# Optimization experiments

Measured on AMD Instinct MI355X. Metric: run time of the kernel, lower is better.

The kernel has to match this reference:

```python
import jax, jax.numpy as jnp
import numpy as np

LN2 = float(np.log(2.0))

def ssp(x):
    # ShiftedSoftplus: softplus(x) - log(2)
    return jax.nn.softplus(x) - LN2

N_NODES = 40000
N_EDGES = 640000
HIDDEN = 128
N_FILTERS = 128
N_GAUSS = 50
CUTOFF = 10.0

def setup_inputs() -> dict:
    key = jax.random.key(0)
    ks = jax.random.split(key, 12)
    s = 0.05
    x = jax.random.normal(ks[0], (N_NODES, HIDDEN), dtype=jnp.float32)
    edge_index = jax.random.randint(ks[1], (2, N_EDGES), 0, N_NODES)
    edge_weight = jax.random.uniform(ks[2], (N_EDGES,), dtype=jnp.float32) * CUTOFF
    edge_attr = jax.random.normal(ks[3], (N_EDGES, N_GAUSS), dtype=jnp.float32)
    # filter MLP params (Linear(num_gaussians,num_filters), ssp, Linear(num_filters,num_filters))
    mlp_w1 = jax.random.normal(ks[4], (N_FILTERS, N_GAUSS), dtype=jnp.float32) * s
    mlp_b1 = jnp.zeros((N_FILTERS,), dtype=jnp.float32)
    mlp_w2 = jax.random.normal(ks[5], (N_FILTERS, N_FILTERS), dtype=jnp.float32) * s
    mlp_b2 = jnp.zeros((N_FILTERS,), dtype=jnp.float32)
    # CFConv linears: lin1 (no bias), lin2 (bias)
    lin1_w = jax.random.normal(ks[6], (N_FILTERS, HIDDEN), dtype=jnp.float32) * s
    lin2_w = jax.random.normal(ks[7], (HIDDEN, N_FILTERS), dtype=jnp.float32) * s
    lin2_b = jnp.zeros((HIDDEN,), dtype=jnp.float32)
    # output linear
    lin_w = jax.random.normal(ks[8], (HIDDEN, HIDDEN), dtype=jnp.float32) * s
    lin_b = jnp.zeros((HIDDEN,), dtype=jnp.float32)
    return {
        "x": x, "edge_index": edge_index, "edge_weight": edge_weight, "edge_attr": edge_attr,
        "mlp_w1": mlp_w1, "mlp_b1": mlp_b1, "mlp_w2": mlp_w2, "mlp_b2": mlp_b2,
        "lin1_w": lin1_w, "lin2_w": lin2_w, "lin2_b": lin2_b,
        "lin_w": lin_w, "lin_b": lin_b,
    }

def reference(x, edge_index, edge_weight, edge_attr,
              mlp_w1, mlp_b1, mlp_w2, mlp_b2,
              lin1_w, lin2_w, lin2_b, lin_w, lin_b):
    src, dst = edge_index[0], edge_index[1]
    # cosine envelope
    C = 0.5 * (jnp.cos(edge_weight * jnp.pi / CUTOFF) + 1.0)  # (E,)
    # filter MLP on Gaussian-smeared distances
    W = ssp(edge_attr @ mlp_w1.T + mlp_b1) @ mlp_w2.T + mlp_b2  # (E, F)
    W = W * C[:, None]
    # CFConv: lin1 -> gather x_j -> multiply -> scatter-add -> lin2
    h = x @ lin1_w.T                                            # (N, F)
    msg = h[src] * W                                            # (E, F)
    agg = jax.ops.segment_sum(msg, dst, num_segments=x.shape[0])  # (N, F)
    h2 = agg @ lin2_w.T + lin2_b                                # (N, H)
    # activation + output projection
    out = ssp(h2) @ lin_w.T + lin_b                             # (N, H)
    return out
```

## Files before the change

### kernel.cpp

```cpp
#include <hip/hip_runtime.h>
#include <math.h>

#define LN2F 0.69314718055994531f

typedef _Float16 v8hf __attribute__((ext_vector_type(8)));
typedef float    v4f  __attribute__((ext_vector_type(4)));

__device__ __forceinline__ float ssp_fast(float x) {
    float e = __expf(-fabsf(x));
    return fmaxf(x, 0.f) + __logf(1.f + e) - LN2F;
}

__global__ __launch_bounds__(256)
void prep_kernel(const float* __restrict__ w1, const float* __restrict__ w2,
                 const float* __restrict__ l1w, const float* __restrict__ l2w,
                 const float* __restrict__ lw,
                 _Float16* __restrict__ w1f, _Float16* __restrict__ w2f,
                 _Float16* __restrict__ l1f, _Float16* __restrict__ l2f,
                 _Float16* __restrict__ lwf)
{
    int idx = blockIdx.x * 256 + threadIdx.x;
    if (idx < 8192) {
        int i = idx & 7, lane = (idx >> 3) & 63, ks = (idx >> 9) & 1, nt = idx >> 10;
        int r = nt * 16 + (lane & 15);
        int k = ks * 32 + (lane >> 4) * 8 + i;
        w1f[idx] = (k < 50) ? (_Float16)w1[r * 50 + k] : (_Float16)0.f;
        return;
    }
    int o = idx - 8192;
    if (o >= 4 * 16384) return;
    int which = o >> 14;
    int p = o & 16383;
    int i = p & 7, lane = (p >> 3) & 63, ks = (p >> 9) & 3, nt = p >> 11;
    int r = nt * 16 + (lane & 15);
    int k = ks * 32 + (lane >> 4) * 8 + i;
    const float* src = (which == 0) ? w2 : (which == 1) ? l1w : (which == 2) ? l2w : lw;
    _Float16* dst   = (which == 0) ? w2f : (which == 1) ? l1f : (which == 2) ? l2f : lwf;
    dst[p] = (_Float16)src[r * 128 + k];
}

__global__ __launch_bounds__(256)
void h_gemm_kernel(const float* __restrict__ X, const _Float16* __restrict__ Wf,
                   float* __restrict__ Y, int M)
{
    const int tid = threadIdx.x, lane = tid & 63, wv = tid >> 6;
    const int l15 = lane & 15, quad = lane >> 4;
    const int mb = blockIdx.x * 64 + wv * 16;
    const int nt0 = blockIdx.y * 4;

    const int mA = (mb + l15 < M) ? (mb + l15) : (M - 1);
    v8hf a[4];
    #pragma unroll
    for (int ks = 0; ks < 4; ++ks) {
        const float4* xp = (const float4*)&X[(size_t)mA * 128 + ks * 32 + quad * 8];
        float4 x0 = xp[0], x1 = xp[1];
        v8hf t = {(_Float16)x0.x, (_Float16)x0.y, (_Float16)x0.z, (_Float16)x0.w,
                  (_Float16)x1.x, (_Float16)x1.y, (_Float16)x1.z, (_Float16)x1.w};
        a[ks] = t;
    }
    #pragma unroll
    for (int nt = nt0; nt < nt0 + 4; ++nt) {
        v4f acc = {0.f, 0.f, 0.f, 0.f};
        #pragma unroll
        for (int ks = 0; ks < 4; ++ks) {
            const v8hf b = *(const v8hf*)&Wf[((nt * 4 + ks) * 64 + lane) * 8];
            acc = __builtin_amdgcn_mfma_f32_16x16x32_f16(a[ks], b, acc, 0, 0, 0);
        }
        const int col = nt * 16 + l15;
        #pragma unroll
        for (int r = 0; r < 4; ++r) {
            int row = mb + quad * 4 + r;
            if (row < M) Y[(size_t)row * 128 + col] = acc[r];
        }
    }
}

__global__ __launch_bounds__(256)
void fused_out_kernel(const float* __restrict__ agg, const _Float16* __restrict__ l2f,
                      const float* __restrict__ l2b, const _Float16* __restrict__ lwf,
                      const float* __restrict__ lb, float* __restrict__ out, int M)
{
    __shared__ __align__(16) _Float16 Sh[64 * 138];
    const int tid = threadIdx.x, lane = tid & 63, wv = tid >> 6;
    const int l15 = lane & 15, quad = lane >> 4;
    const int m0 = wv * 16;
    const int gbase = blockIdx.x * 64;
    const int nt0 = blockIdx.y * 4;

    const int mA = (gbase + m0 + l15 < M) ? (gbase + m0 + l15) : (M - 1);
    v8hf a[4];
    #pragma unroll
    for (int ks = 0; ks < 4; ++ks) {
        const float4* xp = (const float4*)&agg[(size_t)mA * 128 + ks * 32 + quad * 8];
        float4 x0 = xp[0], x1 = xp[1];
        v8hf t = {(_Float16)x0.x, (_Float16)x0.y, (_Float16)x0.z, (_Float16)x0.w,
                  (_Float16)x1.x, (_Float16)x1.y, (_Float16)x1.z, (_Float16)x1.w};
        a[ks] = t;
    }
    #pragma unroll
    for (int nt = 0; nt < 8; ++nt) {
        v4f acc = {0.f, 0.f, 0.f, 0.f};
        #pragma unroll
        for (int ks = 0; ks < 4; ++ks) {
            const v8hf b = *(const v8hf*)&l2f[((nt * 4 + ks) * 64 + lane) * 8];
            acc = __builtin_amdgcn_mfma_f32_16x16x32_f16(a[ks], b, acc, 0, 0, 0);
        }
        const float bj = l2b[nt * 16 + l15];
        #pragma unroll
        for (int r = 0; r < 4; ++r)
            Sh[(m0 + quad * 4 + r) * 138 + nt * 16 + l15] =
                (_Float16)ssp_fast(acc[r] + bj);
    }
    v8hf ua[4];
    #pragma unroll
    for (int ks = 0; ks < 4; ++ks)
        ua[ks] = *(const v8hf*)&Sh[(m0 + l15) * 138 + ks * 32 + quad * 8];

    #pragma unroll
    for (int nt = nt0; nt < nt0 + 4; ++nt) {
        v4f acc = {0.f, 0.f, 0.f, 0.f};
        #pragma unroll
        for (int ks = 0; ks < 4; ++ks) {
            const v8hf b = *(const v8hf*)&lwf[((nt * 4 + ks) * 64 + lane) * 8];
            acc = __builtin_amdgcn_mfma_f32_16x16x32_f16(ua[ks], b, acc, 0, 0, 0);
        }
        const int col = nt * 16 + l15;
        const float bj = lb[col];
        #pragma unroll
        for (int r = 0; r < 4; ++r) {
            int row = gbase + m0 + quad * 4 + r;
            if (row < M) out[(size_t)row * 128 + col] = acc[r] + bj;
        }
    }
}

__global__ __launch_bounds__(256)
void attr16_kernel(const float* __restrict__ attr, _Float16* __restrict__ attrL, int E)
{
    int idx = blockIdx.x * 256 + threadIdx.x;
    const int stride = gridDim.x * 256;
    const int total = E * 8;
    for (; idx < total; idx += stride) {
        const int e = idx >> 3, sub = idx & 7;
        const float* rp = attr + (size_t)e * 50 + sub * 8;
        v8hf t;
        #pragma unroll
        for (int j = 0; j < 8; ++j) {
            const int c = sub * 8 + j;
            t[j] = (c < 50) ? (_Float16)rp[j] : (_Float16)0.f;
        }
        *(v8hf*)&attrL[(size_t)e * 64 + sub * 8] = t;
    }
}

__global__ __launch_bounds__(256)
void rank_hist_kernel(const int* __restrict__ dst, int* __restrict__ cnt,
                      int* __restrict__ rank, int E)
{
    int i = blockIdx.x * 256 + threadIdx.x;
    const int stride = gridDim.x * 256;
    for (; i < E; i += stride) rank[i] = atomicAdd(&cnt[dst[i]], 1);
}

__global__ __launch_bounds__(256)
void scan1_kernel(int* __restrict__ data, int* __restrict__ bsum, int N)
{
    __shared__ int wsum[4];
    const int t = threadIdx.x, lane = t & 63, wv = t >> 6;
    const int base = blockIdx.x * 1024 + t * 4;
    int v0 = 0, v1 = 0, v2 = 0, v3 = 0;
    if (base + 0 < N) v0 = data[base + 0];
    if (base + 1 < N) v1 = data[base + 1];
    if (base + 2 < N) v2 = data[base + 2];
    if (base + 3 < N) v3 = data[base + 3];
    const int s = v0 + v1 + v2 + v3;
    int sc = s;
    #pragma unroll
    for (int d = 1; d < 64; d <<= 1) {
        int o = __shfl_up(sc, d);
        if (lane >= d) sc += o;
    }
    if (lane == 63) wsum[wv] = sc;
    __syncthreads();
    int wo = 0;
    for (int j = 0; j < wv; ++j) wo += wsum[j];
    int run = wo + (sc - s);
    if (base + 0 < N) data[base + 0] = run; run += v0;
    if (base + 1 < N) data[base + 1] = run; run += v1;
    if (base + 2 < N) data[base + 2] = run; run += v2;
    if (base + 3 < N) data[base + 3] = run; run += v3;
    if (t == 255) bsum[blockIdx.x] = wo + sc;
}

__global__ __launch_bounds__(256)
void scan2_kernel(int* __restrict__ offs, const int* __restrict__ bsum, int N, int E)
{
    int add = 0;
    for (int j = 0; j < (int)blockIdx.x; ++j) add += bsum[j];
    const int base = blockIdx.x * 1024 + threadIdx.x * 4;
    #pragma unroll
    for (int r = 0; r < 4; ++r) {
        int i = base + r;
        if (i < N) offs[i] += add;
    }
    if (blockIdx.x == 0 && threadIdx.x == 0) offs[N] = E;
}

__global__ __launch_bounds__(256)
void build_rec_kernel(const int* __restrict__ src, const int* __restrict__ dst,
                      const float* __restrict__ ew, const int* __restrict__ rank,
                      const int* __restrict__ offs, int4* __restrict__ recP, int E)
{
    int i = blockIdx.x * 256 + threadIdx.x;
    const int stride = gridDim.x * 256;
    for (; i < E; i += stride) {
        const int d = dst[i];
        const int slot = offs[d] + rank[i];
        int4 rec;
        rec.x = i;
        rec.y = src[i];
        rec.z = d;
        rec.w = __float_as_int(0.5f * (__cosf(ew[i] * 0.31415926535897932f) + 1.f));
        recP[slot] = rec;
    }
}

__global__ __launch_bounds__(256, 7)
void edge_kernel(const _Float16* __restrict__ attrL,
                 const int4* __restrict__ recP,
                 const _Float16* __restrict__ w1f,
                 const _Float16* __restrict__ w2f,
                 const float* __restrict__ b1,
                 const float* __restrict__ b2,
                 const float* __restrict__ h,
                 float* __restrict__ agg,
                 int E)
{
    __shared__ __align__(16) _Float16 Uh[64 * 138];

    const int tid = threadIdx.x;
    const int e_base = blockIdx.x * 64;
    const int lane = tid & 63, wv = tid >> 6;
    const int m0 = wv * 16, l15 = lane & 15, quad = lane >> 4;

    const int s0 = e_base + m0 + quad * 4;
    int dIdx[4]; float cC[4]; const float* hrow[4]; float* arow[4]; bool val[4];
    #pragma unroll
    for (int r = 0; r < 4; ++r) {
        const int sg = s0 + r;
        val[r] = sg < E;
        const int s = val[r] ? sg : (E - 1);
        const int4 rec = recP[s];
        dIdx[r] = rec.z;
        cC[r] = __int_as_float(rec.w);
        hrow[r] = h + (size_t)rec.y * 128;
        arow[r] = agg + (size_t)rec.z * 128;
    }

    int sA = e_base + m0 + l15;
    if (sA >= E) sA = E - 1;
    const int eidA = ((const int*)recP)[(size_t)sA * 4];
    const _Float16* ap = attrL + (size_t)eidA * 64;
    const v8hf a0 = *(const v8hf*)(ap + quad * 8);
    const v8hf a1 = *(const v8hf*)(ap + 32 + quad * 8);

    float hv[8][4];
    #pragma unroll
    for (int nt = 0; nt < 8; ++nt)
        #pragma unroll
        for (int r = 0; r < 4; ++r)
            hv[nt][r] = hrow[r][nt * 16 + l15];

    #pragma unroll
    for (int nt = 0; nt < 8; ++nt) {
        v4f acc = {0.f, 0.f, 0.f, 0.f};
        const v8hf bA = *(const v8hf*)&w1f[((nt * 2 + 0) * 64 + lane) * 8];
        const v8hf bB = *(const v8hf*)&w1f[((nt * 2 + 1) * 64 + lane) * 8];
        acc = __builtin_amdgcn_mfma_f32_16x16x32_f16(a0, bA, acc, 0, 0, 0);
        acc = __builtin_amdgcn_mfma_f32_16x16x32_f16(a1, bB, acc, 0, 0, 0);
        const float bj = b1[nt * 16 + l15];
        #pragma unroll
        for (int r = 0; r < 4; ++r)
            Uh[(m0 + quad * 4 + r) * 138 + nt * 16 + l15] =
                (_Float16)ssp_fast(acc[r] + bj);
    }

    v8hf ua[4];
    #pragma unroll
    for (int ks = 0; ks < 4; ++ks)
        ua[ks] = *(const v8hf*)&Uh[(m0 + l15) * 138 + ks * 32 + quad * 8];

    #pragma unroll
    for (int nt = 0; nt < 8; ++nt) {
        v4f acc = {0.f, 0.f, 0.f, 0.f};
        #pragma unroll
        for (int ks = 0; ks < 4; ++ks) {
            const v8hf b = *(const v8hf*)&w2f[((nt * 4 + ks) * 64 + lane) * 8];
            acc = __builtin_amdgcn_mfma_f32_16x16x32_f16(ua[ks], b, acc, 0, 0, 0);
        }
        const int col = nt * 16 + l15;
        const float bj = b2[col];
        float m[4];
        #pragma unroll
        for (int r = 0; r < 4; ++r)
            m[r] = val[r] ? (acc[r] + bj) * cC[r] * hv[nt][r] : 0.f;
        float run = m[0];
        #pragma unroll
        for (int r = 1; r < 4; ++r) {
            if (dIdx[r] == dIdx[r - 1]) {
                run += m[r];
            } else {
                atomicAdd(arow[r - 1] + col, run);
                run = m[r];
            }
        }
        atomicAdd(arow[3] + col, run);
    }
}

extern "C" void kernel_launch(void* const* d_in, const int* in_sizes, int n_in,
                              void* d_out, int out_size, void* d_ws, size_t ws_size,
                              hipStream_t stream)
{
    const float* x   = (const float*)d_in[0];
    const int*   ei  = (const int*)  d_in[1];
    const float* ew  = (const float*)d_in[2];
    const float* ea  = (const float*)d_in[3];
    const float* w1  = (const float*)d_in[4];
    const float* b1  = (const float*)d_in[5];
    const float* w2  = (const float*)d_in[6];
    const float* b2  = (const float*)d_in[7];
    const float* l1w = (const float*)d_in[8];
    const float* l2w = (const float*)d_in[9];
    const float* l2b = (const float*)d_in[10];
    const float* lw  = (const float*)d_in[11];
    const float* lb  = (const float*)d_in[12];

    const int N = in_sizes[0] / 128;
    const int E = in_sizes[2];
    const int NB = (N + 1023) / 1024;

    char* base = (char*)d_ws;
    size_t off = 0;
    auto take = [&](size_t bytes) -> char* {
        char* r = base + off;
        off = (off + bytes + 255) & ~(size_t)255;
        return r;
    };
    float*    hbuf  = (float*)   take((size_t)N * 128 * 4);
    float*    agg   = (float*)   take((size_t)N * 128 * 4);
    _Float16* w1f   = (_Float16*)take(8192 * 2);
    _Float16* w2f   = (_Float16*)take(16384 * 2);
    _Float16* l1f   = (_Float16*)take(16384 * 2);
    _Float16* l2f   = (_Float16*)take(16384 * 2);
    _Float16* lwf   = (_Float16*)take(16384 * 2);
    int*      offs  = (int*)     take((size_t)(N + 1) * 4);
    int*      bsum  = (int*)     take((size_t)NB * 4);
    int*      rank  = (int*)     take((size_t)E * 4);
    int4*     recP  = (int4*)    take((size_t)E * 16);
    _Float16* attrL = (_Float16*)take((size_t)E * 64 * 2);

    const int nb = (N + 63) / 64;
    const int eb = (E + 63) / 64;
    const int tb = (E + 255) / 256;

    prep_kernel<<<288, 256, 0, stream>>>(w1, w2, l1w, l2w, lw,
                                         w1f, w2f, l1f, l2f, lwf);
    hipMemsetAsync(agg, 0, (size_t)N * 128 * sizeof(float), stream);
    hipMemsetAsync(offs, 0, (size_t)(N + 1) * sizeof(int), stream);

    attr16_kernel<<<(E * 8 + 255) / 256, 256, 0, stream>>>(ea, attrL, E);
    rank_hist_kernel<<<tb, 256, 0, stream>>>(ei + E, offs, rank, E);
    scan1_kernel<<<NB, 256, 0, stream>>>(offs, bsum, N);
    scan2_kernel<<<NB, 256, 0, stream>>>(offs, bsum, N, E);
    build_rec_kernel<<<tb, 256, 0, stream>>>(ei, ei + E, ew, rank, offs, recP, E);

    h_gemm_kernel<<<dim3(nb, 2), 256, 0, stream>>>(x, l1f, hbuf, N);
    edge_kernel<<<eb, 256, 0, stream>>>(attrL, recP, w1f, w2f, b1, b2,
                                        hbuf, agg, E);
    fused_out_kernel<<<dim3(nb, 2), 256, 0, stream>>>(agg, l2f, l2b, lwf, lb,
                                                      (float*)d_out, N);
}
```

Baseline: 575.2 us.

## Make edge kernel persistent with W2 held in registers and W1 in LDS

Turns the edge kernel into a persistent grid of 512 blocks that loop over 64-edge tiles. Each block loads W1 into shared memory and each lane keeps its W2 fragments (32 v8hf) and the biases in registers once, instead of re-reading them from global memory per tile. Launch bounds drop from 7 to 2 blocks per SM so the much larger register footprint fits. The cost is lower occupancy and less latency hiding for the irregular h gathers and atomics.

```diff
diff --git a/kernel.cpp b/kernel.cpp
--- a/kernel.cpp
+++ b/kernel.cpp
@@ -225,7 +225,7 @@
     }
 }
 
-__global__ __launch_bounds__(256, 7)
+__global__ __launch_bounds__(256, 2)
 void edge_kernel(const _Float16* __restrict__ attrL,
                  const int4* __restrict__ recP,
                  const _Float16* __restrict__ w1f,
@@ -234,87 +234,107 @@
                  const float* __restrict__ b2,
                  const float* __restrict__ h,
                  float* __restrict__ agg,
-                 int E)
-{
+                 int E, int nTiles)
+{
+    __shared__ __align__(16) _Float16 W1s[8192];
     __shared__ __align__(16) _Float16 Uh[64 * 138];
 
     const int tid = threadIdx.x;
-    const int e_base = blockIdx.x * 64;
     const int lane = tid & 63, wv = tid >> 6;
     const int m0 = wv * 16, l15 = lane & 15, quad = lane >> 4;
 
-    const int s0 = e_base + m0 + quad * 4;
-    int dIdx[4]; float cC[4]; const float* hrow[4]; float* arow[4]; bool val[4];
-    #pragma unroll
-    for (int r = 0; r < 4; ++r) {
-        const int sg = s0 + r;
-        val[r] = sg < E;
-        const int s = val[r] ? sg : (E - 1);
-        const int4 rec = recP[s];
-        dIdx[r] = rec.z;
-        cC[r] = __int_as_float(rec.w);
-        hrow[r] = h + (size_t)rec.y * 128;
-        arow[r] = agg + (size_t)rec.z * 128;
-    }
-
-    int sA = e_base + m0 + l15;
-    if (sA >= E) sA = E - 1;
-    const int eidA = ((const int*)recP)[(size_t)sA * 4];
-    const _Float16* ap = attrL + (size_t)eidA * 64;
-    const v8hf a0 = *(const v8hf*)(ap + quad * 8);
-    const v8hf a1 = *(const v8hf*)(ap + 32 + quad * 8);
-
-    float hv[8][4];
-    #pragma unroll
-    for (int nt = 0; nt < 8; ++nt)
-        #pragma unroll
-        for (int r = 0; r < 4; ++r)
-            hv[nt][r] = hrow[r][nt * 16 + l15];
-
+    #pragma unroll
+    for (int i = 0; i < 4; ++i)
+        ((v8hf*)W1s)[tid + 256 * i] = ((const v8hf*)w1f)[tid + 256 * i];
+
+    v8hf w2r[32];
+    #pragma unroll
+    for (int f = 0; f < 32; ++f)
+        w2r[f] = *(const v8hf*)&w2f[((size_t)f * 64 + lane) * 8];
+
+    float b1v[8], b2v[8];
     #pragma unroll
     for (int nt = 0; nt < 8; ++nt) {
-        v4f acc = {0.f, 0.f, 0.f, 0.f};
-        const v8hf bA = *(const v8hf*)&w1f[((nt * 2 + 0) * 64 + lane) * 8];
-        const v8hf bB = *(const v8hf*)&w1f[((nt * 2 + 1) * 64 + lane) * 8];
-        acc = __builtin_amdgcn_mfma_f32_16x16x32_f16(a0, bA, acc, 0, 0, 0);
-        acc = __builtin_amdgcn_mfma_f32_16x16x32_f16(a1, bB, acc, 0, 0, 0);
-        const float bj = b1[nt * 16 + l15];
-        #pragma unroll
-        for (int r = 0; r < 4; ++r)
-            Uh[(m0 + quad * 4 + r) * 138 + nt * 16 + l15] =
-                (_Float16)ssp_fast(acc[r] + bj);
-    }
-
-    v8hf ua[4];
-    #pragma unroll
-    for (int ks = 0; ks < 4; ++ks)
-        ua[ks] = *(const v8hf*)&Uh[(m0 + l15) * 138 + ks * 32 + quad * 8];
-
-    #pragma unroll
-    for (int nt = 0; nt < 8; ++nt) {
-        v4f acc = {0.f, 0.f, 0.f, 0.f};
-        #pragma unroll
-        for (int ks = 0; ks < 4; ++ks) {
-            const v8hf b = *(const v8hf*)&w2f[((nt * 4 + ks) * 64 + lane) * 8];
-            acc = __builtin_amdgcn_mfma_f32_16x16x32_f16(ua[ks], b, acc, 0, 0, 0);
-        }
-        const int col = nt * 16 + l15;
-        const float bj = b2[col];
-        float m[4];
-        #pragma unroll
-        for (int r = 0; r < 4; ++r)
-            m[r] = val[r] ? (acc[r] + bj) * cC[r] * hv[nt][r] : 0.f;
-        float run = m[0];
-        #pragma unroll
-        for (int r = 1; r < 4; ++r) {
-            if (dIdx[r] == dIdx[r - 1]) {
-                run += m[r];
-            } else {
-                atomicAdd(arow[r - 1] + col, run);
-                run = m[r];
+        b1v[nt] = b1[nt * 16 + l15];
+        b2v[nt] = b2[nt * 16 + l15];
+    }
+    __syncthreads();
+
+    for (int tile = blockIdx.x; tile < nTiles; tile += (int)gridDim.x) {
+        const int e_base = tile * 64;
+
+        const int s0 = e_base + m0 + quad * 4;
+        int dIdx[4]; float cC[4]; const float* hrow[4]; float* arow[4]; bool val[4];
+        #pragma unroll
+        for (int r = 0; r < 4; ++r) {
+            const int sg = s0 + r;
+            val[r] = sg < E;
+            const int s = val[r] ? sg : (E - 1);
+            const int4 rec = recP[s];
+            dIdx[r] = rec.z;
+            cC[r] = __int_as_float(rec.w);
+            hrow[r] = h + (size_t)rec.y * 128;
+            arow[r] = agg + (size_t)rec.z * 128;
+        }
+
+        int sA = e_base + m0 + l15;
+        if (sA >= E) sA = E - 1;
+        const int eidA = ((const int*)recP)[(size_t)sA * 4];
+        const _Float16* ap = attrL + (size_t)eidA * 64;
+        const v8hf a0 = *(const v8hf*)(ap + quad * 8);
+        const v8hf a1 = *(const v8hf*)(ap + 32 + quad * 8);
+
+        float hv[8][4];
+        #pragma unroll
+        for (int nt = 0; nt < 8; ++nt)
+            #pragma unroll
+            for (int r = 0; r < 4; ++r)
+                hv[nt][r] = hrow[r][nt * 16 + l15];
+
+        #pragma unroll
+        for (int nt = 0; nt < 8; ++nt) {
+            v4f acc = {0.f, 0.f, 0.f, 0.f};
+            const v8hf bA = *(const v8hf*)&W1s[((nt * 2 + 0) * 64 + lane) * 8];
+            const v8hf bB = *(const v8hf*)&W1s[((nt * 2 + 1) * 64 + lane) * 8];
+            acc = __builtin_amdgcn_mfma_f32_16x16x32_f16(a0, bA, acc, 0, 0, 0);
+            acc = __builtin_amdgcn_mfma_f32_16x16x32_f16(a1, bB, acc, 0, 0, 0);
+            const float bj = b1v[nt];
+            #pragma unroll
+            for (int r = 0; r < 4; ++r)
+                Uh[(m0 + quad * 4 + r) * 138 + nt * 16 + l15] =
+                    (_Float16)ssp_fast(acc[r] + bj);
+        }
+
+        v8hf ua[4];
+        #pragma unroll
+        for (int ks = 0; ks < 4; ++ks)
+            ua[ks] = *(const v8hf*)&Uh[(m0 + l15) * 138 + ks * 32 + quad * 8];
+
+        #pragma unroll
+        for (int nt = 0; nt < 8; ++nt) {
+            v4f acc = {0.f, 0.f, 0.f, 0.f};
+            #pragma unroll
+            for (int ks = 0; ks < 4; ++ks)
+                acc = __builtin_amdgcn_mfma_f32_16x16x32_f16(ua[ks], w2r[nt * 4 + ks],
+                                                             acc, 0, 0, 0);
+            const int col = nt * 16 + l15;
+            const float bj = b2v[nt];
+            float m[4];
+            #pragma unroll
+            for (int r = 0; r < 4; ++r)
+                m[r] = val[r] ? (acc[r] + bj) * cC[r] * hv[nt][r] : 0.f;
+            float run = m[0];
+            #pragma unroll
+            for (int r = 1; r < 4; ++r) {
+                if (dIdx[r] == dIdx[r - 1]) {
+                    run += m[r];
+                } else {
+                    atomicAdd(arow[r - 1] + col, run);
+                    run = m[r];
+                }
             }
-        }
-        atomicAdd(arow[3] + col, run);
+            atomicAdd(arow[3] + col, run);
+        }
     }
 }
 
@@ -361,8 +381,8 @@
     _Float16* attrL = (_Float16*)take((size_t)E * 64 * 2);
 
     const int nb = (N + 63) / 64;
-    const int eb = (E + 63) / 64;
     const int tb = (E + 255) / 256;
+    const int nTiles = (E + 63) / 64;
 
     prep_kernel<<<288, 256, 0, stream>>>(w1, w2, l1w, l2w, lw,
                                          w1f, w2f, l1f, l2f, lwf);
@@ -376,8 +396,8 @@
     build_rec_kernel<<<tb, 256, 0, stream>>>(ei, ei + E, ew, rank, offs, recP, E);
 
     h_gemm_kernel<<<dim3(nb, 2), 256, 0, stream>>>(x, l1f, hbuf, N);
-    edge_kernel<<<eb, 256, 0, stream>>>(attrL, recP, w1f, w2f, b1, b2,
-                                        hbuf, agg, E);
+    edge_kernel<<<512, 256, 0, stream>>>(attrL, recP, w1f, w2f, b1, b2,
+                                         hbuf, agg, E, nTiles);
     fused_out_kernel<<<dim3(nb, 2), 256, 0, stream>>>(agg, l2f, l2b, lwf, lb,
                                                       (float*)d_out, N);
 }
```

Measured after the change: 569.7 us. Within noise of the previous version (-1.0%).

## Fuse attr fp16 conversion with edge permutation into dst-sorted layout

Applied to the files above, without the earlier changes.

The separate attr16 and build_rec kernels are merged into one perm_kernel. It converts edge_attr to fp16 and writes it directly at the dst-sorted slot, alongside the edge record. The edge kernel then reads attributes contiguously by sorted position instead of gathering them through the original edge id. This removes one launch and the indirect gather, but the attr writes become scattered. Separately, h_gemm uses 4 column blocks of 2 tiles each for more parallelism, and edge_kernel's occupancy hint rises to 8.

```diff
diff --git a/kernel.cpp b/kernel.cpp
--- a/kernel.cpp
+++ b/kernel.cpp
@@ -46,7 +46,7 @@
     const int tid = threadIdx.x, lane = tid & 63, wv = tid >> 6;
     const int l15 = lane & 15, quad = lane >> 4;
     const int mb = blockIdx.x * 64 + wv * 16;
-    const int nt0 = blockIdx.y * 4;
+    const int nt0 = blockIdx.y * 2;
 
     const int mA = (mb + l15 < M) ? (mb + l15) : (M - 1);
     v8hf a[4];
@@ -59,7 +59,7 @@
         a[ks] = t;
     }
     #pragma unroll
-    for (int nt = nt0; nt < nt0 + 4; ++nt) {
+    for (int nt = nt0; nt < nt0 + 2; ++nt) {
         v4f acc = {0.f, 0.f, 0.f, 0.f};
         #pragma unroll
         for (int ks = 0; ks < 4; ++ks) {
@@ -131,25 +131,6 @@
             int row = gbase + m0 + quad * 4 + r;
             if (row < M) out[(size_t)row * 128 + col] = acc[r] + bj;
         }
-    }
-}
-
-__global__ __launch_bounds__(256)
-void attr16_kernel(const float* __restrict__ attr, _Float16* __restrict__ attrL, int E)
-{
-    int idx = blockIdx.x * 256 + threadIdx.x;
-    const int stride = gridDim.x * 256;
-    const int total = E * 8;
-    for (; idx < total; idx += stride) {
-        const int e = idx >> 3, sub = idx & 7;
-        const float* rp = attr + (size_t)e * 50 + sub * 8;
-        v8hf t;
-        #pragma unroll
-        for (int j = 0; j < 8; ++j) {
-            const int c = sub * 8 + j;
-            t[j] = (c < 50) ? (_Float16)rp[j] : (_Float16)0.f;
-        }
-        *(v8hf*)&attrL[(size_t)e * 64 + sub * 8] = t;
     }
 }
 
@@ -207,26 +188,39 @@
 }
 
 __global__ __launch_bounds__(256)
-void build_rec_kernel(const int* __restrict__ src, const int* __restrict__ dst,
-                      const float* __restrict__ ew, const int* __restrict__ rank,
-                      const int* __restrict__ offs, int4* __restrict__ recP, int E)
-{
-    int i = blockIdx.x * 256 + threadIdx.x;
+void perm_kernel(const float* __restrict__ attr, const float* __restrict__ ew,
+                 const int* __restrict__ src, const int* __restrict__ dst,
+                 const int* __restrict__ rank, const int* __restrict__ offs,
+                 int4* __restrict__ recP, _Float16* __restrict__ attrP, int E)
+{
+    int idx = blockIdx.x * 256 + threadIdx.x;
     const int stride = gridDim.x * 256;
-    for (; i < E; i += stride) {
-        const int d = dst[i];
-        const int slot = offs[d] + rank[i];
-        int4 rec;
-        rec.x = i;
-        rec.y = src[i];
-        rec.z = d;
-        rec.w = __float_as_int(0.5f * (__cosf(ew[i] * 0.31415926535897932f) + 1.f));
-        recP[slot] = rec;
-    }
-}
-
-__global__ __launch_bounds__(256, 7)
-void edge_kernel(const _Float16* __restrict__ attrL,
+    const int total = E * 8;
+    for (; idx < total; idx += stride) {
+        const int e = idx >> 3, sub = idx & 7;
+        const int d = dst[e];
+        const int slot = offs[d] + rank[e];
+        const float* rp = attr + (size_t)e * 50 + sub * 8;
+        v8hf t;
+        #pragma unroll
+        for (int j = 0; j < 8; ++j) {
+            const int c = sub * 8 + j;
+            t[j] = (c < 50) ? (_Float16)rp[j] : (_Float16)0.f;
+        }
+        *(v8hf*)&attrP[(size_t)slot * 64 + sub * 8] = t;
+        if (sub == 0) {
+            int4 rec;
+            rec.x = src[e];
+            rec.y = d;
+            rec.z = __float_as_int(0.5f * (__cosf(ew[e] * 0.31415926535897932f) + 1.f));
+            rec.w = 0;
+            recP[slot] = rec;
+        }
+    }
+}
+
+__global__ __launch_bounds__(256, 8)
+void edge_kernel(const _Float16* __restrict__ attrP,
                  const int4* __restrict__ recP,
                  const _Float16* __restrict__ w1f,
                  const _Float16* __restrict__ w2f,
@@ -251,16 +245,15 @@
         val[r] = sg < E;
         const int s = val[r] ? sg : (E - 1);
         const int4 rec = recP[s];
-        dIdx[r] = rec.z;
-        cC[r] = __int_as_float(rec.w);
-        hrow[r] = h + (size_t)rec.y * 128;
-        arow[r] = agg + (size_t)rec.z * 128;
+        dIdx[r] = rec.y;
+        cC[r] = __int_as_float(rec.z);
+        hrow[r] = h + (size_t)rec.x * 128;
+        arow[r] = agg + (size_t)rec.y * 128;
     }
 
     int sA = e_base + m0 + l15;
     if (sA >= E) sA = E - 1;
-    const int eidA = ((const int*)recP)[(size_t)sA * 4];
-    const _Float16* ap = attrL + (size_t)eidA * 64;
+    const _Float16* ap = attrP + (size_t)sA * 64;
     const v8hf a0 = *(const v8hf*)(ap + quad * 8);
     const v8hf a1 = *(const v8hf*)(ap + 32 + quad * 8);
 
@@ -358,7 +351,7 @@
     int*      bsum  = (int*)     take((size_t)NB * 4);
     int*      rank  = (int*)     take((size_t)E * 4);
     int4*     recP  = (int4*)    take((size_t)E * 16);
-    _Float16* attrL = (_Float16*)take((size_t)E * 64 * 2);
+    _Float16* attrP = (_Float16*)take((size_t)E * 64 * 2);
 
     const int nb = (N + 63) / 64;
     const int eb = (E + 63) / 64;
@@ -369,14 +362,14 @@
     hipMemsetAsync(agg, 0, (size_t)N * 128 * sizeof(float), stream);
     hipMemsetAsync(offs, 0, (size_t)(N + 1) * sizeof(int), stream);
 
-    attr16_kernel<<<(E * 8 + 255) / 256, 256, 0, stream>>>(ea, attrL, E);
     rank_hist_kernel<<<tb, 256, 0, stream>>>(ei + E, offs, rank, E);
     scan1_kernel<<<NB, 256, 0, stream>>>(offs, bsum, N);
     scan2_kernel<<<NB, 256, 0, stream>>>(offs, bsum, N, E);
-    build_rec_kernel<<<tb, 256, 0, stream>>>(ei, ei + E, ew, rank, offs, recP, E);
-
-    h_gemm_kernel<<<dim3(nb, 2), 256, 0, stream>>>(x, l1f, hbuf, N);
-    edge_kernel<<<eb, 256, 0, stream>>>(attrL, recP, w1f, w2f, b1, b2,
+    perm_kernel<<<(E * 8 + 255) / 256, 256, 0, stream>>>(ea, ew, ei, ei + E,
+                                                         rank, offs, recP, attrP, E);
+
+    h_gemm_kernel<<<dim3(nb, 4), 256, 0, stream>>>(x, l1f, hbuf, N);
+    edge_kernel<<<eb, 256, 0, stream>>>(attrP, recP, w1f, w2f, b1, b2,
                                         hbuf, agg, E);
     fused_out_kernel<<<dim3(nb, 2), 256, 0, stream>>>(agg, l2f, l2b, lwf, lb,
                                                       (float*)d_out, N);
```

New measurement: 608.6 us. 1.06x slower.

## Merge preprocessing kernels into one cooperative grid-synced build kernel

Applied to the files above, without the earlier changes.

Replaces the separate prep, memset, attr conversion, histogram, two-pass scan and record-build launches with a single cooperative kernel of 512 blocks that uses grid.sync between phases. The aim is to remove launch and inter-kernel gap overhead across about eight small launches. The trade-off is grid-wide barriers, a serial bsum scan on one thread, and fewer threads for the bandwidth-bound phases. It also raises the edge kernel's launch_bounds occupancy hint from 7 to 8, and keeps the old multi-kernel path as a fallback if the cooperative launch fails.

```diff
diff --git a/kernel.cpp b/kernel.cpp
--- a/kernel.cpp
+++ b/kernel.cpp
@@ -1,5 +1,8 @@
 #include <hip/hip_runtime.h>
+#include <hip/hip_cooperative_groups.h>
 #include <math.h>
+
+namespace cg = cooperative_groups;
 
 #define LN2F 0.69314718055994531f
 
@@ -11,15 +14,14 @@
     return fmaxf(x, 0.f) + __logf(1.f + e) - LN2F;
 }
 
-__global__ __launch_bounds__(256)
-void prep_kernel(const float* __restrict__ w1, const float* __restrict__ w2,
-                 const float* __restrict__ l1w, const float* __restrict__ l2w,
-                 const float* __restrict__ lw,
-                 _Float16* __restrict__ w1f, _Float16* __restrict__ w2f,
-                 _Float16* __restrict__ l1f, _Float16* __restrict__ l2f,
-                 _Float16* __restrict__ lwf)
-{
-    int idx = blockIdx.x * 256 + threadIdx.x;
+__device__ __forceinline__ void prep_unit(int idx,
+    const float* __restrict__ w1, const float* __restrict__ w2,
+    const float* __restrict__ l1w, const float* __restrict__ l2w,
+    const float* __restrict__ lw,
+    _Float16* __restrict__ w1f, _Float16* __restrict__ w2f,
+    _Float16* __restrict__ l1f, _Float16* __restrict__ l2f,
+    _Float16* __restrict__ lwf)
+{
     if (idx < 8192) {
         int i = idx & 7, lane = (idx >> 3) & 63, ks = (idx >> 9) & 1, nt = idx >> 10;
         int r = nt * 16 + (lane & 15);
@@ -39,99 +41,119 @@
     dst[p] = (_Float16)src[r * 128 + k];
 }
 
-__global__ __launch_bounds__(256)
-void h_gemm_kernel(const float* __restrict__ X, const _Float16* __restrict__ Wf,
-                   float* __restrict__ Y, int M)
-{
-    const int tid = threadIdx.x, lane = tid & 63, wv = tid >> 6;
-    const int l15 = lane & 15, quad = lane >> 4;
-    const int mb = blockIdx.x * 64 + wv * 16;
-    const int nt0 = blockIdx.y * 4;
-
-    const int mA = (mb + l15 < M) ? (mb + l15) : (M - 1);
-    v8hf a[4];
-    #pragma unroll
-    for (int ks = 0; ks < 4; ++ks) {
-        const float4* xp = (const float4*)&X[(size_t)mA * 128 + ks * 32 + quad * 8];
-        float4 x0 = xp[0], x1 = xp[1];
-        v8hf t = {(_Float16)x0.x, (_Float16)x0.y, (_Float16)x0.z, (_Float16)x0.w,
-                  (_Float16)x1.x, (_Float16)x1.y, (_Float16)x1.z, (_Float16)x1.w};
-        a[ks] = t;
-    }
-    #pragma unroll
-    for (int nt = nt0; nt < nt0 + 4; ++nt) {
-        v4f acc = {0.f, 0.f, 0.f, 0.f};
-        #pragma unroll
-        for (int ks = 0; ks < 4; ++ks) {
-            const v8hf b = *(const v8hf*)&Wf[((nt * 4 + ks) * 64 + lane) * 8];
-            acc = __builtin_amdgcn_mfma_f32_16x16x32_f16(a[ks], b, acc, 0, 0, 0);
-        }
-        const int col = nt * 16 + l15;
+__device__ __forceinline__ void attr_unit(int idx, const float* __restrict__ attr,
+                                          _Float16* __restrict__ attrL)
+{
+    const int e = idx >> 3, sub = idx & 7;
+    const float* rp = attr + (size_t)e * 50 + sub * 8;
+    v8hf t;
+    #pragma unroll
+    for (int j = 0; j < 8; ++j) {
+        const int c = sub * 8 + j;
+        t[j] = (c < 50) ? (_Float16)rp[j] : (_Float16)0.f;
+    }
+    *(v8hf*)&attrL[(size_t)e * 64 + sub * 8] = t;
+}
+
+__global__ __launch_bounds__(256)
+void build_kernel(const float* __restrict__ attr, const float* __restrict__ ew,
+                  const int* __restrict__ src, const int* __restrict__ dst,
+                  const float* __restrict__ w1, const float* __restrict__ w2,
+                  const float* __restrict__ l1w, const float* __restrict__ l2w,
+                  const float* __restrict__ lw,
+                  _Float16* __restrict__ w1f, _Float16* __restrict__ w2f,
+                  _Float16* __restrict__ l1f, _Float16* __restrict__ l2f,
+                  _Float16* __restrict__ lwf,
+                  int* __restrict__ cnt, int* __restrict__ rank,
+                  int* __restrict__ bsum, int4* __restrict__ recP,
+                  _Float16* __restrict__ attrL, float* __restrict__ agg,
+                  int N, int E, int nChunks)
+{
+    cg::grid_group grid = cg::this_grid();
+    const int gtid = blockIdx.x * 256 + threadIdx.x;
+    const int gstride = gridDim.x * 256;
+
+    for (int idx = gtid; idx < 73728; idx += gstride)
+        prep_unit(idx, w1, w2, l1w, l2w, lw, w1f, w2f, l1f, l2f, lwf);
+    for (int idx = gtid; idx < E * 8; idx += gstride)
+        attr_unit(idx, attr, attrL);
+    for (int i = gtid; i < N + 1; i += gstride) cnt[i] = 0;
+    const float4 z = make_float4(0.f, 0.f, 0.f, 0.f);
+    float4* aggv = (float4*)agg;
+    for (int i = gtid; i < N * 32; i += gstride) aggv[i] = z;
+    grid.sync();
+
+    for (int i = gtid; i < E; i += gstride) rank[i] = atomicAdd(&cnt[dst[i]], 1);
+    grid.sync();
+
+    if ((int)blockIdx.x < nChunks) {
+        __shared__ int wsum[4];
+        const int t = threadIdx.x, lane = t & 63, wv = t >> 6;
+        const int base = blockIdx.x * 1024 + t * 4;
+        int v0 = 0, v1 = 0, v2 = 0, v3 = 0;
+        if (base + 0 < N) v0 = cnt[base + 0];
+        if (base + 1 < N) v1 = cnt[base + 1];
+        if (base + 2 < N) v2 = cnt[base + 2];
+        if (base + 3 < N) v3 = cnt[base + 3];
+        const int s = v0 + v1 + v2 + v3;
+        int sc = s;
+        #pragma unroll
+        for (int d = 1; d < 64; d <<= 1) {
+            int o = __shfl_up(sc, d);
+            if (lane >= d) sc += o;
+        }
+        if (lane == 63) wsum[wv] = sc;
+        __syncthreads();
+        int wo = 0;
+        for (int j = 0; j < wv; ++j) wo += wsum[j];
+        int run = wo + (sc - s);
+        if (base + 0 < N) cnt[base + 0] = run; run += v0;
+        if (base + 1 < N) cnt[base + 1] = run; run += v1;
+        if (base + 2 < N) cnt[base + 2] = run; run += v2;
+        if (base + 3 < N) cnt[base + 3] = run; run += v3;
+        if (t == 255) bsum[blockIdx.x] = wo + sc;
+    }
+    grid.sync();
+
+    if (gtid == 0) {
+        int acc = 0;
+        for (int j = 0; j < nChunks; ++j) { int v = bsum[j]; bsum[j] = acc; acc += v; }
+    }
+    grid.sync();
+
+    if ((int)blockIdx.x < nChunks) {
+        const int add = bsum[blockIdx.x];
+        const int base = blockIdx.x * 1024 + threadIdx.x * 4;
         #pragma unroll
         for (int r = 0; r < 4; ++r) {
-            int row = mb + quad * 4 + r;
-            if (row < M) Y[(size_t)row * 128 + col] = acc[r];
-        }
-    }
-}
-
-__global__ __launch_bounds__(256)
-void fused_out_kernel(const float* __restrict__ agg, const _Float16* __restrict__ l2f,
-                      const float* __restrict__ l2b, const _Float16* __restrict__ lwf,
-                      const float* __restrict__ lb, float* __restrict__ out, int M)
-{
-    __shared__ __align__(16) _Float16 Sh[64 * 138];
-    const int tid = threadIdx.x, lane = tid & 63, wv = tid >> 6;
-    const int l15 = lane & 15, quad = lane >> 4;
-    const int m0 = wv * 16;
-    const int gbase = blockIdx.x * 64;
-    const int nt0 = blockIdx.y * 4;
-
-    const int mA = (gbase + m0 + l15 < M) ? (gbase + m0 + l15) : (M - 1);
-    v8hf a[4];
-    #pragma unroll
-    for (int ks = 0; ks < 4; ++ks) {
-        const float4* xp = (const float4*)&agg[(size_t)mA * 128 + ks * 32 + quad * 8];
-        float4 x0 = xp[0], x1 = xp[1];
-        v8hf t = {(_Float16)x0.x, (_Float16)x0.y, (_Float16)x0.z, (_Float16)x0.w,
-                  (_Float16)x1.x, (_Float16)x1.y, (_Float16)x1.z, (_Float16)x1.w};
-        a[ks] = t;
-    }
-    #pragma unroll
-    for (int nt = 0; nt < 8; ++nt) {
-        v4f acc = {0.f, 0.f, 0.f, 0.f};
-        #pragma unroll
-        for (int ks = 0; ks < 4; ++ks) {
-            const v8hf b = *(const v8hf*)&l2f[((nt * 4 + ks) * 64 + lane) * 8];
-            acc = __builtin_amdgcn_mfma_f32_16x16x32_f16(a[ks], b, acc, 0, 0, 0);
-        }
-        const float bj = l2b[nt * 16 + l15];
-        #pragma unroll
-        for (int r = 0; r < 4; ++r)
-            Sh[(m0 + quad * 4 + r) * 138 + nt * 16 + l15] =
-                (_Float16)ssp_fast(acc[r] + bj);
-    }
-    v8hf ua[4];
-    #pragma unroll
-    for (int ks = 0; ks < 4; ++ks)
-        ua[ks] = *(const v8hf*)&Sh[(m0 + l15) * 138 + ks * 32 + quad * 8];
-
-    #pragma unroll
-    for (int nt = nt0; nt < nt0 + 4; ++nt) {
-        v4f acc = {0.f, 0.f, 0.f, 0.f};
-        #pragma unroll
-        for (int ks = 0; ks < 4; ++ks) {
-            const v8hf b = *(const v8hf*)&lwf[((nt * 4 + ks) * 64 + lane) * 8];
-            acc = __builtin_amdgcn_mfma_f32_16x16x32_f16(ua[ks], b, acc, 0, 0, 0);
-        }
-        const int col = nt * 16 + l15;
-        const float bj = lb[col];
-        #pragma unroll
-        for (int r = 0; r < 4; ++r) {
-            int row = gbase + m0 + quad * 4 + r;
-            if (row < M) out[(size_t)row * 128 + col] = acc[r] + bj;
-        }
-    }
+            int i = base + r;
+            if (i < N) cnt[i] += add;
+        }
+    }
+    grid.sync();
+
+    for (int i = gtid; i < E; i += gstride) {
+        const int d = dst[i];
+        const int slot = cnt[d] + rank[i];
+        int4 rec;
+        rec.x = i;
+        rec.y = src[i];
+        rec.z = d;
+        rec.w = __float_as_int(0.5f * (__cosf(ew[i] * 0.31415926535897932f) + 1.f));
+        recP[slot] = rec;
+    }
+}
+
+__global__ __launch_bounds__(256)
+void prep_kernel(const float* __restrict__ w1, const float* __restrict__ w2,
+                 const float* __restrict__ l1w, const float* __restrict__ l2w,
+                 const float* __restrict__ lw,
+                 _Float16* __restrict__ w1f, _Float16* __restrict__ w2f,
+                 _Float16* __restrict__ l1f, _Float16* __restrict__ l2f,
+                 _Float16* __restrict__ lwf)
+{
+    int idx = blockIdx.x * 256 + threadIdx.x;
+    prep_unit(idx, w1, w2, l1w, l2w, lw, w1f, w2f, l1f, l2f, lwf);
 }
 
 __global__ __launch_bounds__(256)
@@ -139,18 +161,7 @@
 {
     int idx = blockIdx.x * 256 + threadIdx.x;
     const int stride = gridDim.x * 256;
-    const int total = E * 8;
-    for (; idx < total; idx += stride) {
-        const int e = idx >> 3, sub = idx & 7;
-        const float* rp = attr + (size_t)e * 50 + sub * 8;
-        v8hf t;
-        #pragma unroll
-        for (int j = 0; j < 8; ++j) {
-            const int c = sub * 8 + j;
-            t[j] = (c < 50) ? (_Float16)rp[j] : (_Float16)0.f;
-        }
-        *(v8hf*)&attrL[(size_t)e * 64 + sub * 8] = t;
-    }
+    for (; idx < E * 8; idx += stride) attr_unit(idx, attr, attrL);
 }
 
 __global__ __launch_bounds__(256)
@@ -225,7 +236,102 @@
     }
 }
 
-__global__ __launch_bounds__(256, 7)
+__global__ __launch_bounds__(256)
+void h_gemm_kernel(const float* __restrict__ X, const _Float16* __restrict__ Wf,
+                   float* __restrict__ Y, int M)
+{
+    const int tid = threadIdx.x, lane = tid & 63, wv = tid >> 6;
+    const int l15 = lane & 15, quad = lane >> 4;
+    const int mb = blockIdx.x * 64 + wv * 16;
+    const int nt0 = blockIdx.y * 4;
+
+    const int mA = (mb + l15 < M) ? (mb + l15) : (M - 1);
+    v8hf a[4];
+    #pragma unroll
+    for (int ks = 0; ks < 4; ++ks) {
+        const float4* xp = (const float4*)&X[(size_t)mA * 128 + ks * 32 + quad * 8];
+        float4 x0 = xp[0], x1 = xp[1];
+        v8hf t = {(_Float16)x0.x, (_Float16)x0.y, (_Float16)x0.z, (_Float16)x0.w,
+                  (_Float16)x1.x, (_Float16)x1.y, (_Float16)x1.z, (_Float16)x1.w};
+        a[ks] = t;
+    }
+    #pragma unroll
+    for (int nt = nt0; nt < nt0 + 4; ++nt) {
+        v4f acc = {0.f, 0.f, 0.f, 0.f};
+        #pragma unroll
+        for (int ks = 0; ks < 4; ++ks) {
+            const v8hf b = *(const v8hf*)&Wf[((nt * 4 + ks) * 64 + lane) * 8];
+            acc = __builtin_amdgcn_mfma_f32_16x16x32_f16(a[ks], b, acc, 0, 0, 0);
+        }
+        const int col = nt * 16 + l15;
+        #pragma unroll
+        for (int r = 0; r < 4; ++r) {
+            int row = mb + quad * 4 + r;
+            if (row < M) Y[(size_t)row * 128 + col] = acc[r];
+        }
+    }
+}
+
+__global__ __launch_bounds__(256)
+void fused_out_kernel(const float* __restrict__ agg, const _Float16* __restrict__ l2f,
+                      const float* __restrict__ l2b, const _Float16* __restrict__ lwf,
+                      const float* __restrict__ lb, float* __restrict__ out, int M)
+{
+    __shared__ __align__(16) _Float16 Sh[64 * 138];
+    const int tid = threadIdx.x, lane = tid & 63, wv = tid >> 6;
+    const int l15 = lane & 15, quad = lane >> 4;
+    const int m0 = wv * 16;
+    const int gbase = blockIdx.x * 64;
+    const int nt0 = blockIdx.y * 4;
+
+    const int mA = (gbase + m0 + l15 < M) ? (gbase + m0 + l15) : (M - 1);
+    v8hf a[4];
+    #pragma unroll
+    for (int ks = 0; ks < 4; ++ks) {
+        const float4* xp = (const float4*)&agg[(size_t)mA * 128 + ks * 32 + quad * 8];
+        float4 x0 = xp[0], x1 = xp[1];
+        v8hf t = {(_Float16)x0.x, (_Float16)x0.y, (_Float16)x0.z, (_Float16)x0.w,
+                  (_Float16)x1.x, (_Float16)x1.y, (_Float16)x1.z, (_Float16)x1.w};
+        a[ks] = t;
+    }
+    #pragma unroll
+    for (int nt = 0; nt < 8; ++nt) {
+        v4f acc = {0.f, 0.f, 0.f, 0.f};
+        #pragma unroll
+        for (int ks = 0; ks < 4; ++ks) {
+            const v8hf b = *(const v8hf*)&l2f[((nt * 4 + ks) * 64 + lane) * 8];
+            acc = __builtin_amdgcn_mfma_f32_16x16x32_f16(a[ks], b, acc, 0, 0, 0);
+        }
+        const float bj = l2b[nt * 16 + l15];
+        #pragma unroll
+        for (int r = 0; r < 4; ++r)
+            Sh[(m0 + quad * 4 + r) * 138 + nt * 16 + l15] =
+                (_Float16)ssp_fast(acc[r] + bj);
+    }
+    v8hf ua[4];
+    #pragma unroll
+    for (int ks = 0; ks < 4; ++ks)
+        ua[ks] = *(const v8hf*)&Sh[(m0 + l15) * 138 + ks * 32 + quad * 8];
+
+    #pragma unroll
+    for (int nt = nt0; nt < nt0 + 4; ++nt) {
+        v4f acc = {0.f, 0.f, 0.f, 0.f};
+        #pragma unroll
+        for (int ks = 0; ks < 4; ++ks) {
+            const v8hf b = *(const v8hf*)&lwf[((nt * 4 + ks) * 64 + lane) * 8];
+            acc = __builtin_amdgcn_mfma_f32_16x16x32_f16(ua[ks], b, acc, 0, 0, 0);
+        }
+        const int col = nt * 16 + l15;
+        const float bj = lb[col];
+        #pragma unroll
+        for (int r = 0; r < 4; ++r) {
+            int row = gbase + m0 + quad * 4 + r;
+            if (row < M) out[(size_t)row * 128 + col] = acc[r] + bj;
+        }
+    }
+}
+
+__global__ __launch_bounds__(256, 8)
 void edge_kernel(const _Float16* __restrict__ attrL,
                  const int4* __restrict__ recP,
                  const _Float16* __restrict__ w1f,
@@ -338,7 +444,7 @@
 
     const int N = in_sizes[0] / 128;
     const int E = in_sizes[2];
-    const int NB = (N + 1023) / 1024;
+    const int nChunks = (N + 1023) / 1024;
 
     char* base = (char*)d_ws;
     size_t off = 0;
@@ -354,8 +460,8 @@
     _Float16* l1f   = (_Float16*)take(16384 * 2);
     _Float16* l2f   = (_Float16*)take(16384 * 2);
     _Float16* lwf   = (_Float16*)take(16384 * 2);
-    int*      offs  = (int*)     take((size_t)(N + 1) * 4);
-    int*      bsum  = (int*)     take((size_t)NB * 4);
+    int*      cnt   = (int*)     take((size_t)(N + 1) * 4);
+    int*      bsum  = (int*)     take((size_t)nChunks * 4);
     int*      rank  = (int*)     take((size_t)E * 4);
     int4*     recP  = (int4*)    take((size_t)E * 16);
     _Float16* attrL = (_Float16*)take((size_t)E * 64 * 2);
@@ -364,16 +470,31 @@
     const int eb = (E + 63) / 64;
     const int tb = (E + 255) / 256;
 
-    prep_kernel<<<288, 256, 0, stream>>>(w1, w2, l1w, l2w, lw,
-                                         w1f, w2f, l1f, l2f, lwf);
-    hipMemsetAsync(agg, 0, (size_t)N * 128 * sizeof(float), stream);
-    hipMemsetAsync(offs, 0, (size_t)(N + 1) * sizeof(int), stream);
-
-    attr16_kernel<<<(E * 8 + 255) / 256, 256, 0, stream>>>(ea, attrL, E);
-    rank_hist_kernel<<<tb, 256, 0, stream>>>(ei + E, offs, rank, E);
-    scan1_kernel<<<NB, 256, 0, stream>>>(offs, bsum, N);
-    scan2_kernel<<<NB, 256, 0, stream>>>(offs, bsum, N, E);
-    build_rec_kernel<<<tb, 256, 0, stream>>>(ei, ei + E, ew, rank, offs, recP, E);
+    const int* eiSrc = ei;
+    const int* eiDst = ei + E;
+    int  Nv = N, Ev = E, nCv = nChunks;
+
+    void* args[] = {
+        (void*)&ea, (void*)&ew, (void*)&eiSrc, (void*)&eiDst,
+        (void*)&w1, (void*)&w2, (void*)&l1w, (void*)&l2w, (void*)&lw,
+        (void*)&w1f, (void*)&w2f, (void*)&l1f, (void*)&l2f, (void*)&lwf,
+        (void*)&cnt, (void*)&rank, (void*)&bsum, (void*)&recP,
+        (void*)&attrL, (void*)&agg, (void*)&Nv, (void*)&Ev, (void*)&nCv };
+
+    hipError_t cerr = hipLaunchCooperativeKernel((const void*)build_kernel,
+                                                 dim3(512), dim3(256),
+                                                 args, 0, stream);
+    if (cerr != hipSuccess) {
+        prep_kernel<<<288, 256, 0, stream>>>(w1, w2, l1w, l2w, lw,
+                                             w1f, w2f, l1f, l2f, lwf);
+        hipMemsetAsync(agg, 0, (size_t)N * 128 * sizeof(float), stream);
+        hipMemsetAsync(cnt, 0, (size_t)(N + 1) * sizeof(int), stream);
+        attr16_kernel<<<tb, 256, 0, stream>>>(ea, attrL, E);
+        rank_hist_kernel<<<tb, 256, 0, stream>>>(eiDst, cnt, rank, E);
+        scan1_kernel<<<nChunks, 256, 0, stream>>>(cnt, bsum, N);
+        scan2_kernel<<<nChunks, 256, 0, stream>>>(cnt, bsum, N, E);
+        build_rec_kernel<<<tb, 256, 0, stream>>>(eiSrc, eiDst, ew, rank, cnt, recP, E);
+    }
 
     h_gemm_kernel<<<dim3(nb, 2), 256, 0, stream>>>(x, l1f, hbuf, N);
     edge_kernel<<<eb, 256, 0, stream>>>(attrL, recP, w1f, w2f, b1, b2,
```

Measured after the change: 868.7 us. +51.0%, slower.
